# Kernel tuning notes

Measured on AMD Instinct MI355X. Metric: run time of the kernel, lower is better.

The kernel has to match this reference:

```python
import jax, jax.numpy as jnp
import numpy as np

WINDOW_SIZE = 11
SIGMA = 1.5
C1 = 0.01 ** 2
C2 = 0.03 ** 2


def _gaussian_window(window_size, sigma, channel, dtype):
    x = np.arange(window_size)
    g = np.exp(-((x - window_size // 2) ** 2) / (2.0 * sigma ** 2))
    g = g / g.sum()
    w2d = np.outer(g, g).astype(np.float32)  # [K,K]
    # depthwise kernel: [C, 1, K, K] (OIHW with feature_group_count=C)
    w = np.broadcast_to(w2d, (channel, 1, window_size, window_size))
    return jnp.asarray(w, dtype=dtype)


def _blur(x, window, channel):
    pad = WINDOW_SIZE // 2
    return jax.lax.conv_general_dilated(
        x, window,
        window_strides=(1, 1),
        padding=[(pad, pad), (pad, pad)],
        dimension_numbers=('NCHW', 'OIHW', 'NCHW'),
        feature_group_count=channel,
    )


def setup_inputs() -> dict:
    key = jax.random.key(0)
    k1, k2 = jax.random.split(key)
    shape = (16, 3, 512, 512)
    img1 = jax.random.uniform(k1, shape, dtype=jnp.float32)
    img2 = jax.random.uniform(k2, shape, dtype=jnp.float32)
    return {"img1": img1, "img2": img2}


def reference(img1, img2):
    channel = img1.shape[1]
    window = _gaussian_window(WINDOW_SIZE, SIGMA, channel, img1.dtype)

    mu1 = _blur(img1, window, channel)
    mu2 = _blur(img2, window, channel)
    mu1_sq = mu1 * mu1
    mu2_sq = mu2 * mu2
    mu1_mu2 = mu1 * mu2

    sigma1_sq = _blur(img1 * img1, window, channel) - mu1_sq
    sigma2_sq = _blur(img2 * img2, window, channel) - mu2_sq
    sigma12 = _blur(img1 * img2, window, channel) - mu1_mu2

    ssim_map = ((2.0 * mu1_mu2 + C1) * (2.0 * sigma12 + C2)) / (
        (mu1_sq + mu2_sq + C1) * (sigma1_sq + sigma2_sq + C2))
    return jnp.mean(ssim_map)  # size_average=True
```

## Files before the change

### kernel.cpp

```cpp
#include <hip/hip_runtime.h>
#include <math.h>

typedef float v2 __attribute__((ext_vector_type(2)));

#define SCALE 1073741824.0
#define NPIX 12582912.0
#define C1f 1e-4f
#define C2f 9e-4f

struct Wts {
    float w[11];
    v2 hp[12];
};

__device__ __forceinline__ v2 sp(float x) { v2 r; r.x = x; r.y = x; return r; }
__device__ __forceinline__ v2 f2(v2 a, v2 b, v2 c) {
    return __builtin_elementwise_fma(a, b, c);
}

#define LOADP(Abuf, Bbuf, grow) do {                                        \
    int rc_ = (grow); rc_ = rc_ < 0 ? 0 : (rc_ > 511 ? 511 : rc_);          \
    const float* ra_ = baseA + rc_ * 512;                                   \
    const float* rb_ = baseB + rc_ * 512;                                   \
    _Pragma("unroll") for (int k_ = 0; k_ < 7; ++k_) {                      \
        Abuf[k_] = *(const v2*)(ra_ + off[k_]);                             \
        Bbuf[k_] = *(const v2*)(rb_ + off[k_]);                             \
    } } while (0)

#define HPM(Abuf, Bbuf, PH, mval) do {                                      \
    v2 hS_ = sp(0.f), hD_ = sp(0.f), hP_ = sp(0.f), hM_ = sp(0.f);          \
    _Pragma("unroll") for (int j_ = 0; j_ < 12; ++j_) {                     \
        const int e_ = j_ + 1;                                              \
        const float xa_ = (e_ & 1) ? Abuf[e_ >> 1].y : Abuf[e_ >> 1].x;     \
        const float xb_ = (e_ & 1) ? Bbuf[e_ >> 1].y : Bbuf[e_ >> 1].x;     \
        const float u_ = xa_ + xb_, v_ = xa_ - xb_;                         \
        hS_ = f2(hpl[j_], sp(u_), hS_);                                     \
        hD_ = f2(hpl[j_], sp(v_), hD_);                                     \
        hP_ = f2(hpl[j_], sp(u_ * u_), hP_);                                \
        hM_ = f2(hpl[j_], sp(v_ * v_), hM_);                                \
    }                                                                       \
    const v2 mm_ = sp(mval);                                                \
    rS[PH] = hS_ * mm_; rD[PH] = hD_ * mm_;                                 \
    rP[PH] = hP_ * mm_; rM[PH] = hM_ * mm_; } while (0)

#define VOUTM(PH, vmval) do {                                               \
    v2 S_ = sp(0.f), D_ = sp(0.f), P_ = sp(0.f), M_ = sp(0.f);              \
    _Pragma("unroll") for (int k_ = 0; k_ < 11; ++k_) {                     \
        const int q_ = ((PH) + 1 + k_) % 12;                                \
        const v2 wk_ = sp(W.w[k_]);                                         \
        S_ = f2(wk_, rS[q_], S_); D_ = f2(wk_, rD[q_], D_);                 \
        P_ = f2(wk_, rP[q_], P_); M_ = f2(wk_, rM[q_], M_);                 \
    }                                                                       \
    const v2 ss_ = S_ * S_, dd_ = D_ * D_;                                  \
    const v2 mu12_  = (ss_ - dd_) * sp(0.25f);                              \
    const v2 musq_  = (ss_ + dd_) * sp(0.5f);                               \
    const v2 sig12_ = (P_ - M_) * sp(0.25f) - mu12_;                        \
    const v2 sigsm_ = (P_ + M_) * sp(0.5f) - musq_;                         \
    const v2 num_ = (sp(2.f) * mu12_ + sp(C1f)) * (sp(2.f) * sig12_ + sp(C2f)); \
    const v2 den_ = (musq_ + sp(C1f)) * (sigsm_ + sp(C2f));                 \
    v2 r_;                                                                  \
    r_.x = __builtin_amdgcn_rcpf(den_.x);                                   \
    r_.y = __builtin_amdgcn_rcpf(den_.y);                                   \
    r_ = r_ * (sp(2.f) - den_ * r_);                                        \
    loc = f2(num_ * sp(vmval), r_, loc); } while (0)

#define PSTEP(PH, PAR) do {                                                 \
    const float m_ = (X >= 0 && X < 512) ? 1.f : 0.f;                       \
    if (PAR) { HPM(A1, B1, PH, m_); LOADP(A1, B1, X + 2); }                 \
    else     { HPM(A0, B0, PH, m_); LOADP(A0, B0, X + 2); }                 \
    ++X;                                                                    \
    __builtin_amdgcn_sched_barrier(0); } while (0)

#define MSTEP(PH, PAR) do {                                                 \
    const float vm_ = (X - 6 < 512) ? 1.f : 0.f;                            \
    VOUTM(PH, vm_);                                                         \
    const float m_ = (X < 512) ? 1.f : 0.f;                                 \
    if (PAR) { HPM(A1, B1, PH, m_); LOADP(A1, B1, X + 2); }                 \
    else     { HPM(A0, B0, PH, m_); LOADP(A0, B0, X + 2); }                 \
    ++X;                                                                    \
    __builtin_amdgcn_sched_barrier(0); } while (0)

__global__ __launch_bounds__(256, 2) void ssim_main(
    const float* __restrict__ img1, const float* __restrict__ img2,
    unsigned long long* __restrict__ acc, Wts W)
{
    __shared__ float red[4];
    const int tid = threadIdx.x;
    const int lane = tid & 63;
    const int wv = tid >> 6;
    const int r0 = blockIdx.x * 48;
    const int plane = blockIdx.y;
    const int c = wv * 128 + 2 * lane;

    const float* baseA = img1 + (size_t)plane * 262144;
    const float* baseB = img2 + (size_t)plane * 262144;

    int off[7];
#pragma unroll
    for (int k = 0; k < 7; ++k) {
        int o = c - 6 + 2 * k;
        off[k] = o < 0 ? 0 : (o > 510 ? 510 : o);
    }
    v2 hpl[12];
#pragma unroll
    for (int j = 0; j < 12; ++j) {
        const int col = c - 5 + j;
        hpl[j] = (col >= 0 && col < 512) ? W.hp[j] : sp(0.f);
    }

    v2 rS[12], rD[12], rP[12], rM[12];
    v2 A0[7], B0[7], A1[7], B1[7];
    v2 loc = sp(0.f);

    int X = r0 - 5;
    LOADP(A0, B0, r0 - 5);
    LOADP(A1, B1, r0 - 4);
    __builtin_amdgcn_sched_barrier(0);

    PSTEP(0, 0);  PSTEP(1, 1);  PSTEP(2, 0);  PSTEP(3, 1);
    PSTEP(4, 0);  PSTEP(5, 1);  PSTEP(6, 0);  PSTEP(7, 1);
    PSTEP(8, 0);  PSTEP(9, 1);  PSTEP(10, 0);

    for (int b = 0; b < 4; ++b) {
        MSTEP(11, 1); MSTEP(0, 0);  MSTEP(1, 1);  MSTEP(2, 0);
        MSTEP(3, 1);  MSTEP(4, 0);  MSTEP(5, 1);  MSTEP(6, 0);
        MSTEP(7, 1);  MSTEP(8, 0);  MSTEP(9, 1);  MSTEP(10, 0);
    }

    float l = loc.x + loc.y;
#pragma unroll
    for (int o2 = 32; o2; o2 >>= 1)
        l += __shfl_down(l, o2, 64);
    if (lane == 0) red[wv] = l;
    __syncthreads();
    if (tid == 0) {
        const float bs = red[0] + red[1] + red[2] + red[3];
        const unsigned long long q =
            (unsigned long long)__double2ll_rn((double)bs * SCALE);
        atomicAdd(acc, q);
    }
}

__global__ void ssim_final(const unsigned long long* __restrict__ acc,
                           float* __restrict__ out)
{
    if (threadIdx.x == 0)
        out[0] = (float)((double)(*acc) * (1.0 / SCALE) / NPIX);
}

extern "C" void kernel_launch(void* const* d_in, const int* in_sizes, int n_in,
                              void* d_out, int out_size, void* d_ws, size_t ws_size,
                              hipStream_t stream) {
    const float* img1 = (const float*)d_in[0];
    const float* img2 = (const float*)d_in[1];
    float* out = (float*)d_out;
    unsigned long long* acc = (unsigned long long*)d_ws;

    double g[11], ssum = 0.0;
    for (int i = 0; i < 11; ++i) {
        const double d = (double)(i - 5);
        g[i] = exp(-(d * d) / 4.5);
        ssum += g[i];
    }
    Wts W;
    for (int i = 0; i < 11; ++i) W.w[i] = (float)(g[i] / ssum);
    for (int j = 0; j < 12; ++j) {
        v2 p;
        p.x = (j <= 10) ? W.w[j] : 0.f;
        p.y = (j >= 1) ? W.w[j - 1] : 0.f;
        W.hp[j] = p;
    }

    hipMemsetAsync(d_ws, 0, sizeof(unsigned long long), stream);
    ssim_main<<<dim3(11, 48), 256, 0, stream>>>(img1, img2, acc, W);
    ssim_final<<<1, 64, 0, stream>>>(acc, out);
}
```

Before: 84.36 us.

## Stage image rows through per-wave LDS ring with float4 loads

Each wave now loads rows of both images with coalesced float4 global loads into a 4-slot LDS ring buffer, zero-masking out-of-bounds columns, and reads the horizontal stencil window back from LDS. This replaces the overlapping per-lane v2 global loads and removes the per-lane masked horizontal weights. The row tile shrinks from 48 to 37 output rows, giving more blocks, and launch bounds move to 3 blocks per CU. The block-level reduction is replaced by one atomic per wave. The costs are LDS traffic, more halo recomputation from the shorter tiles, and a ring-slot reuse pattern with no explicit barriers, which relies on lockstep execution within a wave.

```diff
diff --git a/kernel.cpp b/kernel.cpp
--- a/kernel.cpp
+++ b/kernel.cpp
@@ -7,6 +7,8 @@
 #define NPIX 12582912.0
 #define C1f 1e-4f
 #define C2f 9e-4f
+#define SLOTF 288
+#define WAVEF 1376
 
 struct Wts {
     float w[11];
@@ -18,125 +20,151 @@
     return __builtin_elementwise_fma(a, b, c);
 }
 
-#define LOADP(Abuf, Bbuf, grow) do {                                        \
+#define LOADP(P, grow) do {                                                 \
     int rc_ = (grow); rc_ = rc_ < 0 ? 0 : (rc_ > 511 ? 511 : rc_);          \
-    const float* ra_ = baseA + rc_ * 512;                                   \
-    const float* rb_ = baseB + rc_ * 512;                                   \
+    if ((P) == 0)      { r1_0 = *(const float4*)(g1 + rc_ * 512);           \
+                         r2_0 = *(const float4*)(g2 + rc_ * 512); }         \
+    else if ((P) == 1) { r1_1 = *(const float4*)(g1 + rc_ * 512);           \
+                         r2_1 = *(const float4*)(g2 + rc_ * 512); }         \
+    else               { r1_2 = *(const float4*)(g1 + rc_ * 512);           \
+                         r2_2 = *(const float4*)(g2 + rc_ * 512); }         \
+} while (0)
+
+#define SWRP(P, S) do {                                                     \
+    float4 o1_, o2_;                                                        \
+    if ((P) == 0)      { o1_ = r1_0; o2_ = r2_0; }                          \
+    else if ((P) == 1) { o1_ = r1_1; o2_ = r2_1; }                          \
+    else               { o1_ = r1_2; o2_ = r2_2; }                          \
+    o1_.x *= cm1.x; o1_.y *= cm1.y; o1_.z *= cm1.z; o1_.w *= cm1.w;         \
+    o2_.x *= cm2.x; o2_.y *= cm2.y; o2_.z *= cm2.z; o2_.w *= cm2.w;         \
+    *(float4*)(wr1 + (S) * SLOTF) = o1_;                                    \
+    *(float4*)(wr2 + (S) * wr2step) = o2_;                                  \
+} while (0)
+
+#define STEPM(p) do {                                                       \
+    const int t_ = 12 * it + (p);                                           \
+    const int gr_ = r0 - 5 + t_;                                            \
+    v2 a_[7], b_[7];                                                        \
     _Pragma("unroll") for (int k_ = 0; k_ < 7; ++k_) {                      \
-        Abuf[k_] = *(const v2*)(ra_ + off[k_]);                             \
-        Bbuf[k_] = *(const v2*)(rb_ + off[k_]);                             \
-    } } while (0)
-
-#define HPM(Abuf, Bbuf, PH, mval) do {                                      \
-    v2 hS_ = sp(0.f), hD_ = sp(0.f), hP_ = sp(0.f), hM_ = sp(0.f);          \
-    _Pragma("unroll") for (int j_ = 0; j_ < 12; ++j_) {                     \
-        const int e_ = j_ + 1;                                              \
-        const float xa_ = (e_ & 1) ? Abuf[e_ >> 1].y : Abuf[e_ >> 1].x;     \
-        const float xb_ = (e_ & 1) ? Bbuf[e_ >> 1].y : Bbuf[e_ >> 1].x;     \
-        const float u_ = xa_ + xb_, v_ = xa_ - xb_;                         \
-        hS_ = f2(hpl[j_], sp(u_), hS_);                                     \
-        hD_ = f2(hpl[j_], sp(v_), hD_);                                     \
-        hP_ = f2(hpl[j_], sp(u_ * u_), hP_);                                \
-        hM_ = f2(hpl[j_], sp(v_ * v_), hM_);                                \
+        a_[k_] = *(const v2*)(rd + ((p) & 3) * SLOTF + 2 * k_);             \
+        b_[k_] = *(const v2*)(rd + ((p) & 3) * SLOTF + 144 + 2 * k_);       \
     }                                                                       \
-    const v2 mm_ = sp(mval);                                                \
-    rS[PH] = hS_ * mm_; rD[PH] = hD_ * mm_;                                 \
-    rP[PH] = hP_ * mm_; rM[PH] = hM_ * mm_; } while (0)
-
-#define VOUTM(PH, vmval) do {                                               \
-    v2 S_ = sp(0.f), D_ = sp(0.f), P_ = sp(0.f), M_ = sp(0.f);              \
-    _Pragma("unroll") for (int k_ = 0; k_ < 11; ++k_) {                     \
-        const int q_ = ((PH) + 1 + k_) % 12;                                \
-        const v2 wk_ = sp(W.w[k_]);                                         \
-        S_ = f2(wk_, rS[q_], S_); D_ = f2(wk_, rD[q_], D_);                 \
-        P_ = f2(wk_, rP[q_], P_); M_ = f2(wk_, rM[q_], M_);                 \
+    LOADP((p) % 3, gr_ + 4);                                                \
+    {              \
+        v2 S_ = sp(0.f), D_ = sp(0.f), P_ = sp(0.f), M_ = sp(0.f);          \
+        _Pragma("unroll") for (int k_ = 0; k_ < 11; ++k_) {                 \
+            const int q_ = ((p) + 1 + k_) % 12;                             \
+            const v2 wk_ = sp(W.w[k_]);                                     \
+            S_ = f2(wk_, rS[q_], S_); D_ = f2(wk_, rD[q_], D_);             \
+            P_ = f2(wk_, rP[q_], P_); M_ = f2(wk_, rM[q_], M_);             \
+        }                                                                   \
+        const v2 ss_ = S_ * S_, dd_ = D_ * D_;                              \
+        const v2 mu12_  = (ss_ - dd_) * sp(0.25f);                          \
+        const v2 musq_  = (ss_ + dd_) * sp(0.5f);                           \
+        const v2 sig12_ = (P_ - M_) * sp(0.25f) - mu12_;                    \
+        const v2 sigsm_ = (P_ + M_) * sp(0.5f) - musq_;                     \
+        const v2 num_ = (sp(2.f) * mu12_ + sp(C1f)) *                       \
+                        (sp(2.f) * sig12_ + sp(C2f));                       \
+        const v2 den_ = (musq_ + sp(C1f)) * (sigsm_ + sp(C2f));             \
+        v2 r_;                                                              \
+        r_.x = __builtin_amdgcn_rcpf(den_.x);                               \
+        r_.y = __builtin_amdgcn_rcpf(den_.y);                               \
+        r_ = r_ * (sp(2.f) - den_ * r_);                                    \
+        const float vm_ = (t_ >= 11 && (r0 + t_ - 11) < 512) ? 1.f : 0.f;   \
+        loc = f2(num_ * sp(vm_), r_, loc);                                  \
     }                                                                       \
-    const v2 ss_ = S_ * S_, dd_ = D_ * D_;                                  \
-    const v2 mu12_  = (ss_ - dd_) * sp(0.25f);                              \
-    const v2 musq_  = (ss_ + dd_) * sp(0.5f);                               \
-    const v2 sig12_ = (P_ - M_) * sp(0.25f) - mu12_;                        \
-    const v2 sigsm_ = (P_ + M_) * sp(0.5f) - musq_;                         \
-    const v2 num_ = (sp(2.f) * mu12_ + sp(C1f)) * (sp(2.f) * sig12_ + sp(C2f)); \
-    const v2 den_ = (musq_ + sp(C1f)) * (sigsm_ + sp(C2f));                 \
-    v2 r_;                                                                  \
-    r_.x = __builtin_amdgcn_rcpf(den_.x);                                   \
-    r_.y = __builtin_amdgcn_rcpf(den_.y);                                   \
-    r_ = r_ * (sp(2.f) - den_ * r_);                                        \
-    loc = f2(num_ * sp(vmval), r_, loc); } while (0)
-
-#define PSTEP(PH, PAR) do {                                                 \
-    const float m_ = (X >= 0 && X < 512) ? 1.f : 0.f;                       \
-    if (PAR) { HPM(A1, B1, PH, m_); LOADP(A1, B1, X + 2); }                 \
-    else     { HPM(A0, B0, PH, m_); LOADP(A0, B0, X + 2); }                 \
-    ++X;                                                                    \
-    __builtin_amdgcn_sched_barrier(0); } while (0)
-
-#define MSTEP(PH, PAR) do {                                                 \
-    const float vm_ = (X - 6 < 512) ? 1.f : 0.f;                            \
-    VOUTM(PH, vm_);                                                         \
-    const float m_ = (X < 512) ? 1.f : 0.f;                                 \
-    if (PAR) { HPM(A1, B1, PH, m_); LOADP(A1, B1, X + 2); }                 \
-    else     { HPM(A0, B0, PH, m_); LOADP(A0, B0, X + 2); }                 \
-    ++X;                                                                    \
-    __builtin_amdgcn_sched_barrier(0); } while (0)
-
-__global__ __launch_bounds__(256, 2) void ssim_main(
+    {          \
+        v2 hS_ = sp(0.f), hD_ = sp(0.f), hP_ = sp(0.f), hM_ = sp(0.f);      \
+        _Pragma("unroll") for (int j_ = 0; j_ < 12; ++j_) {                 \
+            const int e_ = j_ + 1;             \
+            const float xa_ = (e_ & 1) ? a_[e_ >> 1].y : a_[e_ >> 1].x;     \
+            const float xb_ = (e_ & 1) ? b_[e_ >> 1].y : b_[e_ >> 1].x;     \
+            const float u_ = xa_ + xb_, v_ = xa_ - xb_;                     \
+            hS_ = f2(W.hp[j_], sp(u_), hS_);                                \
+            hD_ = f2(W.hp[j_], sp(v_), hD_);                                \
+            hP_ = f2(W.hp[j_], sp(u_ * u_), hP_);                           \
+            hM_ = f2(W.hp[j_], sp(v_ * v_), hM_);                           \
+        }                                                                   \
+        const float m_ = ((unsigned)gr_ < 512u) ? 1.f : 0.f;                \
+        const v2 mm_ = sp(m_);                                              \
+        rS[(p)] = hS_ * mm_; rD[(p)] = hD_ * mm_;                           \
+        rP[(p)] = hP_ * mm_; rM[(p)] = hM_ * mm_;                           \
+    }                                                                       \
+    SWRP(((p) + 1) % 3, ((p) + 2) & 3);                                     \
+    __builtin_amdgcn_sched_barrier(0);                                      \
+} while (0)
+
+__global__ __launch_bounds__(256, 3) void ssim_main(
     const float* __restrict__ img1, const float* __restrict__ img2,
     unsigned long long* __restrict__ acc, Wts W)
 {
-    __shared__ float red[4];
+    __shared__ float ldsbuf[4 * WAVEF];
+
     const int tid = threadIdx.x;
     const int lane = tid & 63;
     const int wv = tid >> 6;
-    const int r0 = blockIdx.x * 48;
+    const int r0 = blockIdx.x * 37;
     const int plane = blockIdx.y;
-    const int c = wv * 128 + 2 * lane;
+    const int wc = wv * 128;
+    const int c = wc + 2 * lane;
 
     const float* baseA = img1 + (size_t)plane * 262144;
     const float* baseB = img2 + (size_t)plane * 262144;
-
-    int off[7];
+    float* ldsW = ldsbuf + wv * WAVEF;
+
+    const int ch1 = (lane < 36) ? lane : (lane - 36);
+    const int cb1 = wc - 8 + 4 * ch1;
+    const int cc1 = cb1 < 0 ? 0 : (cb1 > 508 ? 508 : cb1);
+    const float* g1 = ((lane < 36) ? baseA : baseB) + cc1;
+    float* wr1 = ldsW + ((lane < 36) ? 4 * ch1 : 144 + 4 * ch1);
+    float4 cm1;
+    cm1.x = (cb1 + 0 >= 0 && cb1 + 0 < 512) ? 1.f : 0.f;
+    cm1.y = (cb1 + 1 >= 0 && cb1 + 1 < 512) ? 1.f : 0.f;
+    cm1.z = (cb1 + 2 >= 0 && cb1 + 2 < 512) ? 1.f : 0.f;
+    cm1.w = (cb1 + 3 >= 0 && cb1 + 3 < 512) ? 1.f : 0.f;
+    const bool real2 = (lane < 8);
+    const int ch2 = real2 ? (28 + lane) : 35;
+    const int cb2 = wc - 8 + 4 * ch2;
+    const int cc2 = cb2 < 0 ? 0 : (cb2 > 508 ? 508 : cb2);
+    const float* g2 = baseB + cc2;
+    float* wr2 = ldsW + (real2 ? (144 + 4 * ch2) : (4 * SLOTF + 4 * (lane - 8)));
+    const int wr2step = real2 ? SLOTF : 0;
+    float4 cm2;
+    cm2.x = (real2 && cb2 + 0 >= 0 && cb2 + 0 < 512) ? 1.f : 0.f;
+    cm2.y = (real2 && cb2 + 1 >= 0 && cb2 + 1 < 512) ? 1.f : 0.f;
+    cm2.z = (real2 && cb2 + 2 >= 0 && cb2 + 2 < 512) ? 1.f : 0.f;
+    cm2.w = (real2 && cb2 + 3 >= 0 && cb2 + 3 < 512) ? 1.f : 0.f;
+
+    const float* rd = ldsW + 2 * lane + 2;
+
+    v2 rS[12], rD[12], rP[12], rM[12];
 #pragma unroll
-    for (int k = 0; k < 7; ++k) {
-        int o = c - 6 + 2 * k;
-        off[k] = o < 0 ? 0 : (o > 510 ? 510 : o);
-    }
-    v2 hpl[12];
-#pragma unroll
-    for (int j = 0; j < 12; ++j) {
-        const int col = c - 5 + j;
-        hpl[j] = (col >= 0 && col < 512) ? W.hp[j] : sp(0.f);
-    }
-
-    v2 rS[12], rD[12], rP[12], rM[12];
-    v2 A0[7], B0[7], A1[7], B1[7];
+    for (int q = 0; q < 12; ++q) {
+        rS[q] = sp(0.f); rD[q] = sp(0.f);
+        rP[q] = sp(0.f); rM[q] = sp(0.f);
+    }
     v2 loc = sp(0.f);
-
-    int X = r0 - 5;
-    LOADP(A0, B0, r0 - 5);
-    LOADP(A1, B1, r0 - 4);
+    float4 r1_0, r2_0, r1_1, r2_1, r1_2, r2_2;
+
+    LOADP(0, r0 - 5);  SWRP(0, 0);
+    LOADP(1, r0 - 4);  SWRP(1, 1);
+    LOADP(1, r0 - 3);
+    LOADP(2, r0 - 2);
     __builtin_amdgcn_sched_barrier(0);
 
-    PSTEP(0, 0);  PSTEP(1, 1);  PSTEP(2, 0);  PSTEP(3, 1);
-    PSTEP(4, 0);  PSTEP(5, 1);  PSTEP(6, 0);  PSTEP(7, 1);
-    PSTEP(8, 0);  PSTEP(9, 1);  PSTEP(10, 0);
-
-    for (int b = 0; b < 4; ++b) {
-        MSTEP(11, 1); MSTEP(0, 0);  MSTEP(1, 1);  MSTEP(2, 0);
-        MSTEP(3, 1);  MSTEP(4, 0);  MSTEP(5, 1);  MSTEP(6, 0);
-        MSTEP(7, 1);  MSTEP(8, 0);  MSTEP(9, 1);  MSTEP(10, 0);
+    for (int it = 0; it < 4; ++it) {
+        STEPM(0);  STEPM(1);  STEPM(2);  STEPM(3);
+        STEPM(4);  STEPM(5);  STEPM(6);  STEPM(7);
+        STEPM(8);  STEPM(9);  STEPM(10); STEPM(11);
     }
 
     float l = loc.x + loc.y;
 #pragma unroll
     for (int o2 = 32; o2; o2 >>= 1)
         l += __shfl_down(l, o2, 64);
-    if (lane == 0) red[wv] = l;
-    __syncthreads();
-    if (tid == 0) {
-        const float bs = red[0] + red[1] + red[2] + red[3];
+    if (lane == 0) {
         const unsigned long long q =
-            (unsigned long long)__double2ll_rn((double)bs * SCALE);
+            (unsigned long long)__double2ll_rn((double)l * SCALE);
         atomicAdd(acc, q);
     }
 }
@@ -172,6 +200,6 @@
     }
 
     hipMemsetAsync(d_ws, 0, sizeof(unsigned long long), stream);
-    ssim_main<<<dim3(11, 48), 256, 0, stream>>>(img1, img2, acc, W);
+    ssim_main<<<dim3(14, 48), 256, 0, stream>>>(img1, img2, acc, W);
     ssim_final<<<1, 64, 0, stream>>>(acc, out);
 }
```

Result: slower. 140.2 us (+66.2%).
